# Kernel tuning notes

Hardware: AMD Instinct MI355X
Metric: run time of the kernel (lower is better)

Reference implementation:

```python
import jax, jax.numpy as jnp
import numpy as np

LEVEL = 3  # matches init_kwargs
# pywt Wavelet('db4').rec_lo (synthesis low-pass, 8 taps)
REC_LO = np.array([
    0.23037781330885523, 0.7148465705525415, 0.6308807679295904,
    -0.02798376941698385, -0.18703481171888114, 0.030841381835986965,
    0.032883011666982945, -0.010597401784997278], dtype=np.float32)


def _rec_filters():
    rec_lo = jnp.asarray(REC_LO)
    L = rec_lo.shape[0]
    # QMF relation: rec_hi[k] = (-1)^k * rec_lo[L-1-k]
    signs = jnp.asarray((-1.0) ** np.arange(L), dtype=rec_lo.dtype)
    rec_hi = rec_lo[::-1] * signs
    return rec_lo, rec_hi


def _iswt(coeffs, rec_lo, rec_hi):
    """Inverse stationary (undecimated / a-trous) wavelet transform.

    coeffs = [cA_L, cD_L, cD_{L-1}, ..., cD_1], each of shape [BN, T].
    Perfect reconstruction for the circular-padded dilated-conv SWT
    (ptwt/pywt convention): at each level with dilation d,
      x[n] = 0.5 * sum_m rec_lo[m]*a[(n - d*(m - L//2 + 1)) % T]
                 + rec_hi[m]*cd[(n - d*(m - L//2 + 1)) % T]
    """
    L = rec_lo.shape[0]
    n_lev = len(coeffs) - 1
    res = coeffs[0]
    for c_pos in range(n_lev):
        hi = coeffs[1 + c_pos]
        d = 2 ** (n_lev - 1 - c_pos)
        acc = jnp.zeros_like(res)
        for m in range(L):  # static 8-tap loop, unrolled under jit
            shift = d * (m - L // 2 + 1)
            acc = acc + rec_lo[m] * jnp.roll(res, shift, axis=-1) \
                      + rec_hi[m] * jnp.roll(hi, shift, axis=-1)
        res = 0.5 * acc
    return res


def setup_inputs() -> dict:
    key = jax.random.key(0)
    B, N, T = 32, 64, 4096
    x = jax.random.normal(key, (B, (LEVEL + 1) * N, T), dtype=jnp.float32)
    return {"x": x}


def reference(x):
    B, expanded_N, T = x.shape
    N = expanded_N // (LEVEL + 1)
    xr = x.reshape(B * N, LEVEL + 1, T)  # (B,N,level+1,T) merged over B,N
    coeffs = [xr[:, i, :] for i in range(LEVEL + 1)]
    rec_lo, rec_hi = _rec_filters()
    rec = _iswt(coeffs, rec_lo, rec_hi)  # [B*N, T]
    return rec.reshape(B, N, T)
```

## Files before the change

kernel.cpp:

```cpp
#include <hip/hip_runtime.h>


namespace {

constexpr int TT = 4096;
constexpr int T4 = TT / 4;
constexpr int NT = 256;

template <int D, bool LAST>
__device__ __forceinline__ void iswt_level(const float4* __restrict__ gsrc,
                                           float* lds_res, float* lds_hi,
                                           float4* __restrict__ dst4, int t) {
  constexpr float LO[8] = {
      0.23037781330885523f,  0.7148465705525415f,  0.6308807679295904f,
      -0.02798376941698385f, -0.18703481171888114f, 0.030841381835986965f,
      0.032883011666982945f, -0.010597401784997278f};
  constexpr float HI[8] = {
      -0.010597401784997278f, -0.032883011666982945f, 0.030841381835986965f,
      0.18703481171888114f,   -0.02798376941698385f,  -0.6308807679295904f,
      0.7148465705525415f,    -0.23037781330885523f};

  float4* hiw4 = reinterpret_cast<float4*>(lds_hi);
#pragma unroll
  for (int k = 0; k < 4; ++k) hiw4[t + k * NT] = gsrc[t + k * NT];
  __syncthreads();

  constexpr int W4 = (7 * D + 7) / 4;
  const float4* res4 = reinterpret_cast<const float4*>(lds_res);
  const float4* hir4 = reinterpret_cast<const float4*>(lds_hi);

  float4 acc[4];
#pragma unroll
  for (int g = 0; g < 4; ++g) {
    const int c = t + g * NT;
    float w[4 * W4];

#pragma unroll
    for (int i = 0; i < W4; ++i) {
      const float4 v = res4[(c - D + i) & (T4 - 1)];
      w[4 * i + 0] = v.x; w[4 * i + 1] = v.y;
      w[4 * i + 2] = v.z; w[4 * i + 3] = v.w;
    }
    float a0 = 0.f, a1 = 0.f, a2 = 0.f, a3 = 0.f;
#pragma unroll
    for (int m = 0; m < 8; ++m) {
      const int o = D * (7 - m);
      a0 += LO[m] * w[o + 0];
      a1 += LO[m] * w[o + 1];
      a2 += LO[m] * w[o + 2];
      a3 += LO[m] * w[o + 3];
    }

#pragma unroll
    for (int i = 0; i < W4; ++i) {
      const float4 v = hir4[(c - D + i) & (T4 - 1)];
      w[4 * i + 0] = v.x; w[4 * i + 1] = v.y;
      w[4 * i + 2] = v.z; w[4 * i + 3] = v.w;
    }
#pragma unroll
    for (int m = 0; m < 8; ++m) {
      const int o = D * (7 - m);
      a0 += HI[m] * w[o + 0];
      a1 += HI[m] * w[o + 1];
      a2 += HI[m] * w[o + 2];
      a3 += HI[m] * w[o + 3];
    }
    acc[g] = make_float4(0.5f * a0, 0.5f * a1, 0.5f * a2, 0.5f * a3);
  }

  __syncthreads();
#pragma unroll
  for (int g = 0; g < 4; ++g) dst4[t + g * NT] = acc[g];
  if (!LAST) __syncthreads();
}

__global__ __launch_bounds__(NT) void iswt_kernel(const float* __restrict__ x,
                                                  float* __restrict__ out) {
  __shared__ __align__(16) float lds_res[TT];
  __shared__ __align__(16) float lds_hi[TT];

  const int t = threadIdx.x;
  const int row = blockIdx.x;

  const float4* xr4 = reinterpret_cast<const float4*>(x) + (size_t)row * 4 * T4;
  float4* res4 = reinterpret_cast<float4*>(lds_res);

#pragma unroll
  for (int k = 0; k < 4; ++k) res4[t + k * NT] = xr4[t + k * NT];

  iswt_level<4, false>(xr4 + 1 * T4, lds_res, lds_hi, res4, t);
  iswt_level<2, false>(xr4 + 2 * T4, lds_res, lds_hi, res4, t);
  float4* out4 = reinterpret_cast<float4*>(out) + (size_t)row * T4;
  iswt_level<1, true>(xr4 + 3 * T4, lds_res, lds_hi, out4, t);
}

}

extern "C" void kernel_launch(void* const* d_in, const int* in_sizes, int n_in,
                              void* d_out, int out_size, void* d_ws, size_t ws_size,
                              hipStream_t stream) {
  const float* x = reinterpret_cast<const float*>(d_in[0]);
  float* out = reinterpret_cast<float*>(d_out);
  const int rows = out_size / TT;
  iswt_kernel<<<rows, NT, 0, stream>>>(x, out);
}
```

Before: 202.9 us.

## Prefetch next-level coefficients into registers, compute 16 contiguous outputs per thread with swizzled LDS

```diff
diff --git a/kernel.cpp b/kernel.cpp
--- a/kernel.cpp
+++ b/kernel.cpp
@@ -7,91 +7,114 @@
 constexpr int T4 = TT / 4;
 constexpr int NT = 256;
 
-template <int D, bool LAST>
-__device__ __forceinline__ void iswt_level(const float4* __restrict__ gsrc,
-                                           float* lds_res, float* lds_hi,
-                                           float4* __restrict__ dst4, int t) {
-  constexpr float LO[8] = {
-      0.23037781330885523f,  0.7148465705525415f,  0.6308807679295904f,
-      -0.02798376941698385f, -0.18703481171888114f, 0.030841381835986965f,
-      0.032883011666982945f, -0.010597401784997278f};
-  constexpr float HI[8] = {
-      -0.010597401784997278f, -0.032883011666982945f, 0.030841381835986965f,
-      0.18703481171888114f,   -0.02798376941698385f,  -0.6308807679295904f,
-      0.7148465705525415f,    -0.23037781330885523f};
+__device__ __forceinline__ int swz(int f) { return f ^ ((f >> 3) & 7); }
 
-  float4* hiw4 = reinterpret_cast<float4*>(lds_hi);
-#pragma unroll
-  for (int k = 0; k < 4; ++k) hiw4[t + k * NT] = gsrc[t + k * NT];
-  __syncthreads();
+__constant__ const float LO[8] = {
+    0.23037781330885523f,  0.7148465705525415f,   0.6308807679295904f,
+    -0.02798376941698385f, -0.18703481171888114f, 0.030841381835986965f,
+    0.032883011666982945f, -0.010597401784997278f};
+__constant__ const float HI[8] = {
+    -0.010597401784997278f, -0.032883011666982945f, 0.030841381835986965f,
+    0.18703481171888114f,   -0.02798376941698385f,  -0.6308807679295904f,
+    0.7148465705525415f,    -0.23037781330885523f};
 
-  constexpr int W4 = (7 * D + 7) / 4;
-  const float4* res4 = reinterpret_cast<const float4*>(lds_res);
-  const float4* hir4 = reinterpret_cast<const float4*>(lds_hi);
-
-  float4 acc[4];
-#pragma unroll
-  for (int g = 0; g < 4; ++g) {
-    const int c = t + g * NT;
-    float w[4 * W4];
+template <int D>
+__device__ __forceinline__ void compute_level(const float4* __restrict__ A,
+                                              const float4* __restrict__ B,
+                                              int t, float* __restrict__ a) {
+  constexpr int W = (7 * D + 16 + 3) / 4;
+  const int base = 4 * t - D;
+  float w[4 * W];
 
 #pragma unroll
-    for (int i = 0; i < W4; ++i) {
-      const float4 v = res4[(c - D + i) & (T4 - 1)];
-      w[4 * i + 0] = v.x; w[4 * i + 1] = v.y;
-      w[4 * i + 2] = v.z; w[4 * i + 3] = v.w;
-    }
-    float a0 = 0.f, a1 = 0.f, a2 = 0.f, a3 = 0.f;
+  for (int i = 0; i < W; ++i) {
+    const float4 v = A[swz((base + i) & (T4 - 1))];
+    w[4 * i + 0] = v.x; w[4 * i + 1] = v.y;
+    w[4 * i + 2] = v.z; w[4 * i + 3] = v.w;
+  }
 #pragma unroll
-    for (int m = 0; m < 8; ++m) {
-      const int o = D * (7 - m);
-      a0 += LO[m] * w[o + 0];
-      a1 += LO[m] * w[o + 1];
-      a2 += LO[m] * w[o + 2];
-      a3 += LO[m] * w[o + 3];
-    }
+  for (int j = 0; j < 16; ++j) a[j] = 0.f;
+#pragma unroll
+  for (int m = 0; m < 8; ++m) {
+    const int o = (7 - m) * D;
+#pragma unroll
+    for (int j = 0; j < 16; ++j) a[j] += LO[m] * w[o + j];
+  }
 
 #pragma unroll
-    for (int i = 0; i < W4; ++i) {
-      const float4 v = hir4[(c - D + i) & (T4 - 1)];
-      w[4 * i + 0] = v.x; w[4 * i + 1] = v.y;
-      w[4 * i + 2] = v.z; w[4 * i + 3] = v.w;
-    }
+  for (int i = 0; i < W; ++i) {
+    const float4 v = B[swz((base + i) & (T4 - 1))];
+    w[4 * i + 0] = v.x; w[4 * i + 1] = v.y;
+    w[4 * i + 2] = v.z; w[4 * i + 3] = v.w;
+  }
 #pragma unroll
-    for (int m = 0; m < 8; ++m) {
-      const int o = D * (7 - m);
-      a0 += HI[m] * w[o + 0];
-      a1 += HI[m] * w[o + 1];
-      a2 += HI[m] * w[o + 2];
-      a3 += HI[m] * w[o + 3];
-    }
-    acc[g] = make_float4(0.5f * a0, 0.5f * a1, 0.5f * a2, 0.5f * a3);
+  for (int m = 0; m < 8; ++m) {
+    const int o = (7 - m) * D;
+#pragma unroll
+    for (int j = 0; j < 16; ++j) a[j] += HI[m] * w[o + j];
   }
-
-  __syncthreads();
 #pragma unroll
-  for (int g = 0; g < 4; ++g) dst4[t + g * NT] = acc[g];
-  if (!LAST) __syncthreads();
+  for (int j = 0; j < 16; ++j) a[j] *= 0.5f;
 }
 
-__global__ __launch_bounds__(NT) void iswt_kernel(const float* __restrict__ x,
-                                                  float* __restrict__ out) {
-  __shared__ __align__(16) float lds_res[TT];
-  __shared__ __align__(16) float lds_hi[TT];
+__device__ __forceinline__ void stage(float4* dst, const float4* r, int t) {
+#pragma unroll
+  for (int k = 0; k < 4; ++k) dst[swz(t + k * NT)] = r[k];
+}
+
+__device__ __forceinline__ void writeback(float4* A, const float* a, int t) {
+#pragma unroll
+  for (int j = 0; j < 4; ++j)
+    A[swz(4 * t + j)] =
+        make_float4(a[4 * j + 0], a[4 * j + 1], a[4 * j + 2], a[4 * j + 3]);
+}
+
+__global__ __launch_bounds__(NT, 4) void iswt_kernel(
+    const float* __restrict__ x, float* __restrict__ out) {
+  __shared__ float4 A[T4];
+  __shared__ float4 B[T4];
 
   const int t = threadIdx.x;
   const int row = blockIdx.x;
 
-  const float4* xr4 = reinterpret_cast<const float4*>(x) + (size_t)row * 4 * T4;
-  float4* res4 = reinterpret_cast<float4*>(lds_res);
+  const float4* xr = reinterpret_cast<const float4*>(x) + (size_t)row * 4 * T4;
+
+  float4 rA[4], rB[4];
+#pragma unroll
+  for (int k = 0; k < 4; ++k) rA[k] = xr[0 * T4 + t + k * NT];
+#pragma unroll
+  for (int k = 0; k < 4; ++k) rB[k] = xr[1 * T4 + t + k * NT];
+  stage(A, rA, t);
+  stage(B, rB, t);
+  __syncthreads();
+
+  float4 rH[4];
+#pragma unroll
+  for (int k = 0; k < 4; ++k) rH[k] = xr[2 * T4 + t + k * NT];
+
+  float a[16];
+  compute_level<4>(A, B, t, a);
+  __syncthreads();
+  writeback(A, a, t);
+  stage(B, rH, t);
+  __syncthreads();
 
 #pragma unroll
-  for (int k = 0; k < 4; ++k) res4[t + k * NT] = xr4[t + k * NT];
+  for (int k = 0; k < 4; ++k) rH[k] = xr[3 * T4 + t + k * NT];
 
-  iswt_level<4, false>(xr4 + 1 * T4, lds_res, lds_hi, res4, t);
-  iswt_level<2, false>(xr4 + 2 * T4, lds_res, lds_hi, res4, t);
-  float4* out4 = reinterpret_cast<float4*>(out) + (size_t)row * T4;
-  iswt_level<1, true>(xr4 + 3 * T4, lds_res, lds_hi, out4, t);
+  compute_level<2>(A, B, t, a);
+  __syncthreads();
+  writeback(A, a, t);
+  stage(B, rH, t);
+  __syncthreads();
+
+  compute_level<1>(A, B, t, a);
+
+  float4* o4 = reinterpret_cast<float4*>(out) + (size_t)row * T4;
+#pragma unroll
+  for (int j = 0; j < 4; ++j)
+    o4[4 * t + j] =
+        make_float4(a[4 * j + 0], a[4 * j + 1], a[4 * j + 2], a[4 * j + 3]);
 }
 
 }
```

Result: slower. 209.0 us (+3.0%).
